# Performance work log

Measured on AMD Instinct MI355X. Metric: run time of the kernel, lower is better.

Reference implementation:

```python
import jax, jax.numpy as jnp
import numpy as np

EPS_PROJ = 4e-3   # geoopt float32 ball projection eps
ATANH_EPS = 1e-7

def artanh(x):
    return jnp.arctanh(jnp.clip(x, -1.0 + ATANH_EPS, 1.0 - ATANH_EPS))

def project(x):
    norm = jnp.linalg.norm(x, axis=-1, keepdims=True)
    maxnorm = 1.0 - EPS_PROJ
    return jnp.where(norm > maxnorm, x * (maxnorm / jnp.maximum(norm, 1e-15)), x)

def expmap0(u):
    un = jnp.linalg.norm(u, axis=-1, keepdims=True)
    return jnp.tanh(un) * u / jnp.maximum(un, 1e-15)

def mobius_add(x, y):
    x2 = jnp.sum(x * x, -1, keepdims=True)
    y2 = jnp.sum(y * y, -1, keepdims=True)
    xy = jnp.sum(x * y, -1, keepdims=True)
    num = (1 + 2 * xy + y2) * x + (1 - x2) * y
    den = 1 + 2 * xy + x2 * y2
    return num / jnp.maximum(den, 1e-15)

def mobius_matvec(W, x):
    xn = jnp.linalg.norm(x, axis=-1, keepdims=True)
    mx = x @ W.T
    mxn = jnp.linalg.norm(mx, axis=-1, keepdims=True)
    res = jnp.tanh(mxn / jnp.maximum(xn, 1e-15) * artanh(xn)) * (mx / jnp.maximum(mxn, 1e-15))
    return jnp.where(mxn == 0, jnp.zeros_like(res), res)

def mobius_linear(x, W, b):
    # hyperbolic_input=True, hyperbolic bias, nonlin=None
    return project(mobius_add(mobius_matvec(W, x), b))

def mobius_scalar_mul(r, t):
    tn = jnp.linalg.norm(t, axis=-1, keepdims=True)
    return jnp.tanh(r * artanh(tn)) * (t / jnp.maximum(tn, 1e-15))

def pair_dist(ht, hs):
    # Poincare dist (c=1): 2*artanh(||(-x) mobius_add y||); closed form via GEMM
    x2 = jnp.sum(ht * ht, -1)                    # (b,t)
    y2 = jnp.sum(hs * hs, -1)                    # (b,s)
    xy = jnp.einsum('btd,bsd->bts', ht, hs)      # (b,t,s)
    diff2 = jnp.maximum(x2[:, :, None] + y2[:, None, :] - 2 * xy, 0.0)
    den = jnp.maximum(1 - 2 * xy + x2[:, :, None] * y2[:, None, :], 1e-15)
    return 2.0 * artanh(jnp.sqrt(diff2 / den))


def setup_inputs() -> dict:
    key = jax.random.key(0)
    ks = jax.random.split(key, 7)
    B, T, S, D = 8, 2048, 2048, 128
    source = project(expmap0(0.5 * jax.random.normal(ks[0], (B, T, D), jnp.float32)))
    memory_bank = project(expmap0(0.5 * jax.random.normal(ks[1], (B, S, D), jnp.float32)))
    W_out = 0.01 * jax.random.normal(ks[2], (D, 2 * D), jnp.float32)
    b_out = expmap0(0.25 * jax.random.normal(ks[3], (D,), jnp.float32))
    beta_w = 0.01 * jax.random.normal(ks[4], (1, 1), jnp.float32)
    beta_b = expmap0(0.25 * jax.random.normal(ks[5], (1,), jnp.float32))
    memory_lengths = jax.random.randint(ks[6], (B,), S // 2, S + 1).astype(jnp.int64)
    return {"source": source, "memory_bank": memory_bank, "W_out": W_out,
            "b_out": b_out, "beta_w": beta_w, "beta_b": beta_b,
            "memory_lengths": memory_lengths}


def reference(source, memory_bank, W_out, b_out, beta_w, beta_b, memory_lengths):
    B, T, D = source.shape
    S = memory_bank.shape[1]
    # --- score: -beta(dist(h_t_i, h_s_j)) over all (i,j), vectorized ---
    d = pair_dist(source, memory_bank)[..., None]        # (b,t,s,1)
    align = -mobius_linear(d, beta_w, beta_b)[..., 0]     # (b,t,s)
    # --- length masking ---
    mask = jnp.arange(S) < memory_lengths[:, None]        # (b,s)
    align = jnp.where(mask[:, None, :], align, -jnp.inf)
    align_vectors = jax.nn.softmax(align, axis=-1)        # (b,t,s)
    # --- mobius weighted midpoint over src dim (reducedim=[2]) ---
    y2 = jnp.sum(memory_bank * memory_bank, -1)           # (b,s)
    gamma = 2.0 / jnp.maximum(1.0 - y2, 1e-15)            # lambda_x, k=-1
    den = jnp.einsum('bts,bs->bt', align_vectors, gamma - 1.0)
    den = jnp.where(den >= 0, jnp.maximum(den, 1e-10), jnp.minimum(den, -1e-10))
    nom = jnp.einsum('bts,bs,bsd->btd', align_vectors, gamma, memory_bank)
    cvec = mobius_scalar_mul(0.5, nom / den[..., None])   # (b,t,d)
    # --- output mobius linear on concat, attn_type='hype' => no tanh ---
    concat_c = jnp.concatenate([cvec, source], axis=-1)   # (b,t,2d)
    attn_h = mobius_linear(concat_c, W_out, b_out)        # (b,t,d)
    return attn_h.transpose(1, 0, 2), align_vectors.transpose(1, 0, 2)
```

## Files before the change

### kernel.cpp

```cpp
#include <hip/hip_runtime.h>
#include <stdint.h>

#define B_ 8
#define T_ 2048
#define S_ 2048
#define D_ 128
#define CAP_ 1024

typedef __attribute__((ext_vector_type(8))) short short8;
typedef __attribute__((ext_vector_type(4))) float f32x4;

#define MAXN_ (1.0f - 0.004f)
#define CLIP1_ 0.99999988f

__device__ __forceinline__ unsigned short f2bf(float f) {
    unsigned int u = __builtin_bit_cast(unsigned int, f);
    u += 0x7fffu + ((u >> 16) & 1u);
    return (unsigned short)(u >> 16);
}
__device__ __forceinline__ unsigned int pack2(float a, float b) {
    return (unsigned int)f2bf(a) | ((unsigned int)f2bf(b) << 16);
}
__device__ __forceinline__ float bf2f(unsigned short u) {
    return __builtin_bit_cast(float, ((unsigned int)u) << 16);
}
__device__ __forceinline__ float tanh_fast(float x) {
    float e = __expf(-2.f * fabsf(x));
    float r = (1.f - e) / (1.f + e);
    return copysignf(r, x);
}
__device__ __forceinline__ float atanh_clip(float x) {
    x = fminf(x, CLIP1_);
    return 0.5f * __logf((1.f + x) / (1.f - x));
}
__device__ __forceinline__ float ep_from_av(float av, float w, float bbs, float b2s) {
    float mv = tanh_fast(w * av);
    float ab = mv * bbs;
    float m2 = mv * mv;
    float num = (1.f + 2.f * ab + b2s) * mv + (1.f - m2) * bbs;
    float dd2 = 1.f + 2.f * ab + m2 * b2s;
    float ma = num / fmaxf(dd2, 1e-15f);
    float am = fabsf(ma);
    if (am > MAXN_) ma = ma * (MAXN_ / fmaxf(am, 1e-15f));
    return __expf(-ma);
}
__device__ __forceinline__ float sat_ep(float w, float bbs) {
    return ep_from_av(atanh_clip(2.f), w, bbs, bbs * bbs);
}
__device__ __forceinline__ int get_len(const int* mlen, int b) {
    int is64 = (mlen[1] == 0);
    return is64 ? mlen[2 * b] : mlen[b];
}

__global__ __launch_bounds__(256) void k_prep(
    const float* __restrict__ src, const float* __restrict__ mem,
    const float* __restrict__ Wout, const int* __restrict__ mlen,
    unsigned short* __restrict__ srcb, unsigned short* __restrict__ memb,
    float* __restrict__ x2a, float* __restrict__ y2a,
    unsigned short* __restrict__ Wb, float* __restrict__ gpart,
    float* __restrict__ nbpart, unsigned int* __restrict__ cnt)
{
    __shared__ unsigned short cc_l[128][128];
    __shared__ float gam_l[128];
    __shared__ float gm1_l[128];
    __shared__ float nb_l[2][128];

    const int bid = blockIdx.x;
    const int tid = threadIdx.x;

    if (bid < 256) {
        const bool ismem = bid >= 128;
        const float* inp = ismem ? mem : src;
        unsigned short* outp = ismem ? memb : srcb;
        float* na = ismem ? y2a : x2a;
        const int row0 = (bid & 127) * 128;
        const int lr = tid >> 1;
        const int r = row0 + lr;
        const int ch = (tid & 1) * 64;

        float4 v[16];
        float sq = 0.f;
        const float* rp = inp + (size_t)r * D_ + ch;
        #pragma unroll
        for (int i = 0; i < 16; ++i) {
            v[i] = *(const float4*)(rp + 4 * i);
            sq += v[i].x * v[i].x + v[i].y * v[i].y + v[i].z * v[i].z + v[i].w * v[i].w;
        }
        sq += __shfl_xor(sq, 1);
        unsigned short* op = outp + (size_t)r * D_ + ch;
        #pragma unroll
        for (int i = 0; i < 8; ++i) {
            uint4 pk;
            pk.x = pack2(v[2 * i].x, v[2 * i].y);
            pk.y = pack2(v[2 * i].z, v[2 * i].w);
            pk.z = pack2(v[2 * i + 1].x, v[2 * i + 1].y);
            pk.w = pack2(v[2 * i + 1].z, v[2 * i + 1].w);
            *(uint4*)(op + 8 * i) = pk;
            if (ismem) *(uint4*)&cc_l[lr][ch + 8 * i] = pk;
        }
        if ((tid & 1) == 0) {
            na[r] = sq;
            if (ismem) {
                int b = r >> 11;
                int lenb = get_len(mlen, b);
                bool vld = (r & 2047) < lenb;
                float gam = vld ? 2.f / fmaxf(1.f - sq, 1e-15f) : 0.f;
                gam_l[lr] = gam;
                gm1_l[lr] = vld ? (gam - 1.f) : 0.f;
            }
        }
        if (ismem) {
            __syncthreads();
            const int slot = bid - 128;
            const int c = tid & 127;
            const int h = tid >> 7;
            float acc = 0.f;
            #pragma unroll 8
            for (int r2 = h * 64; r2 < h * 64 + 64; ++r2)
                acc += gam_l[r2] * bf2f(cc_l[r2][c]);
            nb_l[h][c] = acc;
            __syncthreads();
            if (tid < 128)
                nbpart[slot * 128 + tid] = nb_l[0][tid] + nb_l[1][tid];
            if (tid < 64) {
                float g = gm1_l[tid] + gm1_l[tid + 64];
                g += __shfl_xor(g, 1); g += __shfl_xor(g, 2);
                g += __shfl_xor(g, 4); g += __shfl_xor(g, 8);
                g += __shfl_xor(g, 16); g += __shfl_xor(g, 32);
                if (tid == 0) gpart[slot] = g;
            }
        }
    } else {
        if (bid == 256 && tid == 0) *cnt = 0u;
        const int idx0 = (bid - 256) * 4096 + tid * 16;
        float4 v0 = *(const float4*)(Wout + idx0);
        float4 v1 = *(const float4*)(Wout + idx0 + 4);
        float4 v2 = *(const float4*)(Wout + idx0 + 8);
        float4 v3 = *(const float4*)(Wout + idx0 + 12);
        uint4 p0, p1;
        p0.x = pack2(v0.x, v0.y); p0.y = pack2(v0.z, v0.w);
        p0.z = pack2(v1.x, v1.y); p0.w = pack2(v1.z, v1.w);
        p1.x = pack2(v2.x, v2.y); p1.y = pack2(v2.z, v2.w);
        p1.z = pack2(v3.x, v3.y); p1.w = pack2(v3.z, v3.w);
        *(uint4*)(Wb + idx0) = p0;
        *(uint4*)(Wb + idx0 + 8) = p1;
    }
}

__global__ __launch_bounds__(256, 2) void k_score(
    const unsigned short* __restrict__ srcb, const unsigned short* __restrict__ memb,
    const float* __restrict__ x2a, const float* __restrict__ y2a,
    const float* __restrict__ bw, const float* __restrict__ bbp,
    const int* __restrict__ mlen,
    unsigned int* __restrict__ cnt, unsigned int* __restrict__ listR,
    unsigned int* __restrict__ listS, float* __restrict__ listEp,
    float* __restrict__ alignp)
{
    __shared__ unsigned short xs[128][136];
    __shared__ unsigned short ys[128][136];
    __shared__ float x2s[128], y2s[128];
    __shared__ int len_l[8];
    __shared__ float pv_l[8];

    const int tid = threadIdx.x;
    const int blk = blockIdx.x;
    const int b = blk & 7;
    const int rr = blk >> 3;
    const int tt = rr & 15;
    const int st = rr >> 4;
    const int t0 = tt * 128, s0 = st * 128;
    const int lane = tid & 63, wave = tid >> 6;
    const int l15 = lane & 15, q = lane >> 4;
    const int wr = wave >> 1, wc = wave & 1;

    const unsigned short* xg = srcb + ((size_t)(b * T_ + t0)) * D_;
    const unsigned short* yg = memb + ((size_t)(b * S_ + s0)) * D_;
    #pragma unroll
    for (int i = 0; i < 8; ++i) {
        int c = i * 256 + tid;
        int row = c >> 4, off = (c & 15) * 8;
        *(uint4*)&xs[row][off] = *(const uint4*)(xg + (size_t)c * 8);
        *(uint4*)&ys[row][off] = *(const uint4*)(yg + (size_t)c * 8);
    }
    if (tid < 128) { x2s[tid] = x2a[b * T_ + t0 + tid]; y2s[tid] = y2a[b * S_ + s0 + tid]; }
    if (tid < 8) {
        int lv = get_len(mlen, tid);
        len_l[tid] = lv;
        pv_l[tid] = 1.f / (float)lv;
    }
    __syncthreads();

    {
        const int base_f4 = blk * 4096;
        #pragma unroll
        for (int i = 0; i < 16; ++i) {
            int f4 = base_f4 + i * 256 + tid;
            int r = f4 >> 9;
            int b2 = r & 7;
            int s4 = (f4 & 511) << 2;
            int lv = len_l[b2];
            float pvv = pv_l[b2];
            float4 o;
            o.x = (s4 + 0 < lv) ? pvv : 0.f;
            o.y = (s4 + 1 < lv) ? pvv : 0.f;
            o.z = (s4 + 2 < lv) ? pvv : 0.f;
            o.w = (s4 + 3 < lv) ? pvv : 0.f;
            *(float4*)(alignp + (size_t)f4 * 4) = o;
        }
    }

    f32x4 acc[4][4];
    #pragma unroll
    for (int m = 0; m < 4; ++m)
        #pragma unroll
        for (int n = 0; n < 4; ++n)
            acc[m][n] = (f32x4){0.f, 0.f, 0.f, 0.f};

    #pragma unroll
    for (int ki = 0; ki < 4; ++ki) {
        short8 af[4], bf[4];
        #pragma unroll
        for (int m = 0; m < 4; ++m)
            af[m] = *(const short8*)&xs[wr * 64 + m * 16 + l15][ki * 32 + q * 8];
        #pragma unroll
        for (int n = 0; n < 4; ++n)
            bf[n] = *(const short8*)&ys[wc * 64 + n * 16 + l15][ki * 32 + q * 8];
        #pragma unroll
        for (int m = 0; m < 4; ++m)
            #pragma unroll
            for (int n = 0; n < 4; ++n)
                acc[m][n] = __builtin_amdgcn_mfma_f32_16x16x32_bf16(af[m], bf[n], acc[m][n], 0, 0, 0);
    }

    const int lenb = len_l[b];

    float us = tanh_fast(0.5f * CLIP1_);
    const float RSAT = us * us;
    float x2r[16];
    #pragma unroll
    for (int m = 0; m < 4; ++m)
        #pragma unroll
        for (int rg = 0; rg < 4; ++rg)
            x2r[m * 4 + rg] = x2s[wr * 64 + m * 16 + q * 4 + rg];

    unsigned long long um = 0ull;
    #pragma unroll
    for (int n = 0; n < 4; ++n) {
        int col = wc * 64 + n * 16 + l15;
        bool valid = (s0 + col) < lenb;
        float y2v = y2s[col];
        #pragma unroll
        for (int m = 0; m < 4; ++m) {
            #pragma unroll
            for (int rg = 0; rg < 4; ++rg) {
                float xy = acc[m][n][rg];
                float x2v = x2r[m * 4 + rg];
                float diff2 = x2v + y2v - 2.f * xy;
                float dden = fmaf(x2v, y2v, 1.f) - 2.f * xy;
                bool unsat = valid && (diff2 < RSAT * dden);
                um |= ((unsigned long long)unsat) << (n * 16 + m * 4 + rg);
            }
        }
    }

    if (__ballot(um != 0ull)) {
        const float w = bw[0];
        const float bbs = bbp[0];
        const float b2s = bbs * bbs;
        for (int n = 0; n < 4; ++n) {
            int col = wc * 64 + n * 16 + l15;
            for (int m = 0; m < 4; ++m) {
                for (int rg = 0; rg < 4; ++rg) {
                    if (!(um & (1ull << (n * 16 + m * 4 + rg)))) continue;
                    int row = wr * 64 + m * 16 + q * 4 + rg;
                    float xy = acc[m][n][rg];
                    float x2v = x2r[m * 4 + rg];
                    float y2v = y2s[col];
                    float diff2 = fmaxf(x2v + y2v - 2.f * xy, 0.f);
                    float dden = fmaxf(fmaf(x2v, y2v, 1.f) - 2.f * xy, 1e-15f);
                    float u = fminf(sqrtf(diff2 / dden), CLIP1_);
                    float dp = __logf((1.f + u) / (1.f - u));
                    float ep = ep_from_av(atanh_clip(dp), w, bbs, b2s);
                    int rix = b * T_ + t0 + row;
                    unsigned int idx = atomicAdd(cnt, 1u);
                    if (idx < CAP_) {
                        listR[idx] = (unsigned int)rix;
                        listS[idx] = (unsigned int)(b * S_ + s0 + col);
                        listEp[idx] = ep;
                    }
                }
            }
        }
    }
}

__global__ __launch_bounds__(256, 1) void k_out(
    const float* __restrict__ src, const float* __restrict__ mem,
    const unsigned short* __restrict__ Wb, const float* __restrict__ bvec,
    const float* __restrict__ bw, const float* __restrict__ bbp,
    const int* __restrict__ mlen, const float* __restrict__ gpart,
    const float* __restrict__ nbpart, const float* __restrict__ y2a,
    const unsigned int* __restrict__ cnt, const unsigned int* __restrict__ listR,
    const unsigned int* __restrict__ listS, const float* __restrict__ listEp,
    float* __restrict__ attnp, float* __restrict__ alignp)
{
    __shared__ unsigned short W_l[128][264];
    __shared__ unsigned short cc_l[64][264];
    __shared__ float b_l[128];
    __shared__ float nombase_l[128];
    __shared__ float nomn2_l[64], srcn2_l[64], cs_l[64], xn_l[64];
    __shared__ float redA[64], redB[64];
    __shared__ float fA_l[64], fB_l[64];
    __shared__ float bb2_l, Gb_l;

    const int tid = threadIdx.x;
    const int b = blockIdx.x & 7;
    const int tt = blockIdx.x >> 3;
    const int t0 = tt * 64;
    const int lane = tid & 63;
    const int wave = tid >> 6;
    const int l15 = lane & 15;
    const int q = lane >> 4;

    const float epsat = sat_ep(bw[0], bbp[0]);
    const int lenb = get_len(mlen, b);
    unsigned int nc = *cnt; if (nc > CAP_) nc = CAP_;

    #pragma unroll
    for (int i = 0; i < 16; ++i) {
        int c = i * 256 + tid;
        int row = c >> 5, off = (c & 31) * 8;
        *(uint4*)&W_l[row][off] = *(const uint4*)(Wb + (size_t)c * 8);
    }
    if (tid < 128) b_l[tid] = bvec[tid];
    if (tid < 64) { redA[tid] = 0.f; redB[tid] = 0.f; }
    if (tid < 128) {
        float s = 0.f;
        #pragma unroll
        for (int j = 0; j < 16; ++j) s += nbpart[(b * 16 + j) * 128 + tid];
        nombase_l[tid] = s;
    }
    if (tid == 128) {
        float g = 0.f;
        #pragma unroll
        for (int j = 0; j < 16; ++j) g += gpart[b * 16 + j];
        Gb_l = g;
    }
    if (tid == 129) {
        float s = 0.f;
        for (int j = 0; j < 128; ++j) { float v = bvec[j]; s += v * v; }
        bb2_l = s;
    }
    __syncthreads();

    const int r_s = tid >> 2;
    const int d0 = (tid & 3) * 32;
    float4 nv[8], sv[8];
    {
        #pragma unroll
        for (int i = 0; i < 8; ++i) {
            nv[i].x = epsat * nombase_l[d0 + 4 * i + 0];
            nv[i].y = epsat * nombase_l[d0 + 4 * i + 1];
            nv[i].z = epsat * nombase_l[d0 + 4 * i + 2];
            nv[i].w = epsat * nombase_l[d0 + 4 * i + 3];
        }
        if (nc) {
            int myrix = b * T_ + t0 + r_s;
            for (unsigned int i = 0; i < nc; ++i) {
                if ((int)listR[i] != myrix) continue;
                unsigned int sg = listS[i];
                float y2v = y2a[sg];
                float gam = 2.f / fmaxf(1.f - y2v, 1e-15f);
                float cg = (listEp[i] - epsat) * gam;
                const float* yrow = mem + (size_t)sg * D_ + d0;
                #pragma unroll
                for (int k2 = 0; k2 < 8; ++k2) {
                    float4 yv = *(const float4*)(yrow + 4 * k2);
                    nv[k2].x += cg * yv.x; nv[k2].y += cg * yv.y;
                    nv[k2].z += cg * yv.z; nv[k2].w += cg * yv.w;
                }
            }
        }
        size_t sbase = ((size_t)(b * T_ + t0 + r_s)) * D_ + d0;
        float nn = 0.f, ss = 0.f;
        #pragma unroll
        for (int i = 0; i < 8; ++i) {
            sv[i] = *(const float4*)(src + sbase + 4 * i);
            nn += nv[i].x * nv[i].x + nv[i].y * nv[i].y + nv[i].z * nv[i].z + nv[i].w * nv[i].w;
            ss += sv[i].x * sv[i].x + sv[i].y * sv[i].y + sv[i].z * sv[i].z + sv[i].w * sv[i].w;
        }
        nn += __shfl_xor(nn, 1); nn += __shfl_xor(nn, 2);
        ss += __shfl_xor(ss, 1); ss += __shfl_xor(ss, 2);
        if ((tid & 3) == 0) { nomn2_l[r_s] = nn; srcn2_l[r_s] = ss; }
    }
    __syncthreads();

    if (tid < 64) {
        int myrix = b * T_ + t0 + tid;
        float Lv = epsat * (float)lenb;
        float Gv = epsat * Gb_l;
        if (nc) {
            for (unsigned int i = 0; i < nc; ++i) {
                if ((int)listR[i] != myrix) continue;
                float dep = listEp[i] - epsat;
                float y2v = y2a[listS[i]];
                float gam = 2.f / fmaxf(1.f - y2v, 1e-15f);
                Lv += dep;
                Gv += dep * (gam - 1.f);
            }
        }
        float dv = Gv / Lv;
        dv = (dv >= 0.f) ? fmaxf(dv, 1e-10f) : fminf(dv, -1e-10f);
        float Z = Lv * dv;
        float nn2 = nomn2_l[tid];
        float tn = sqrtf(nn2) / fabsf(Z);
        float f = tanh_fast(0.5f * atanh_clip(tn));
        float cs = f / (fmaxf(tn, 1e-15f) * Z);
        cs_l[tid] = cs;
        xn_l[tid] = sqrtf(cs * cs * nn2 + srcn2_l[tid]);
    }
    __syncthreads();

    {
        float cs = cs_l[r_s];
        #pragma unroll
        for (int i = 0; i < 8; ++i) {
            uint2 pk;
            pk.x = pack2(nv[i].x * cs, nv[i].y * cs);
            pk.y = pack2(nv[i].z * cs, nv[i].w * cs);
            *(uint2*)&cc_l[r_s][d0 + 4 * i] = pk;
            uint2 ps;
            ps.x = pack2(sv[i].x, sv[i].y);
            ps.y = pack2(sv[i].z, sv[i].w);
            *(uint2*)&cc_l[r_s][128 + d0 + 4 * i] = ps;
        }
    }
    __syncthreads();

    f32x4 acc[4][2];
    #pragma unroll
    for (int m = 0; m < 4; ++m)
        #pragma unroll
        for (int n = 0; n < 2; ++n)
            acc[m][n] = (f32x4){0.f, 0.f, 0.f, 0.f};
    #pragma unroll
    for (int ki = 0; ki < 8; ++ki) {
        short8 af[4], bf[2];
        #pragma unroll
        for (int m = 0; m < 4; ++m)
            af[m] = *(const short8*)&cc_l[m * 16 + l15][ki * 32 + q * 8];
        #pragma unroll
        for (int n = 0; n < 2; ++n)
            bf[n] = *(const short8*)&W_l[wave * 32 + n * 16 + l15][ki * 32 + q * 8];
        #pragma unroll
        for (int m = 0; m < 4; ++m)
            #pragma unroll
            for (int n = 0; n < 2; ++n)
                acc[m][n] = __builtin_amdgcn_mfma_f32_16x16x32_bf16(af[m], bf[n], acc[m][n], 0, 0, 0);
    }

    float bj[2];
    #pragma unroll
    for (int n = 0; n < 2; ++n) bj[n] = b_l[wave * 32 + n * 16 + l15];

    #pragma unroll
    for (int m = 0; m < 4; ++m) {
        #pragma unroll
        for (int rg = 0; rg < 4; ++rg) {
            int row = m * 16 + q * 4 + rg;
            float pA = 0.f, pB = 0.f;
            #pragma unroll
            for (int n = 0; n < 2; ++n) {
                float v = acc[m][n][rg];
                pA += v * v;
                pB += v * bj[n];
            }
            pA += __shfl_xor(pA, 1); pB += __shfl_xor(pB, 1);
            pA += __shfl_xor(pA, 2); pB += __shfl_xor(pB, 2);
            pA += __shfl_xor(pA, 4); pB += __shfl_xor(pB, 4);
            pA += __shfl_xor(pA, 8); pB += __shfl_xor(pB, 8);
            if (l15 == 0) {
                atomicAdd(&redA[row], pA);
                atomicAdd(&redB[row], pB);
            }
        }
    }
    __syncthreads();

    if (tid < 64) {
        float mxn2 = redA[tid];
        float mxb = redB[tid];
        float xn = xn_l[tid];
        float atx = atanh_clip(xn);
        float mxn = sqrtf(mxn2);
        float scg = tanh_fast(mxn / fmaxf(xn, 1e-15f) * atx) / fmaxf(mxn, 1e-15f);
        float res2 = scg * scg * mxn2;
        float xyb = scg * mxb;
        float b2v = bb2_l;
        float c1 = 1.f + 2.f * xyb + b2v;
        float c2 = 1.f - res2;
        float dd = fmaxf(1.f + 2.f * xyb + res2 * b2v, 1e-15f);
        float nn = sqrtf(fmaxf(c1 * c1 * res2 + 2.f * c1 * c2 * xyb + c2 * c2 * b2v, 0.f)) / dd;
        float rho = (nn > MAXN_) ? (MAXN_ / fmaxf(nn, 1e-15f)) : 1.f;
        fA_l[tid] = rho * c1 * scg / dd;
        fB_l[tid] = rho * c2 / dd;
    }
    __syncthreads();

    #pragma unroll
    for (int m = 0; m < 4; ++m) {
        #pragma unroll
        for (int n = 0; n < 2; ++n) {
            int col = wave * 32 + n * 16 + l15;
            #pragma unroll
            for (int rg = 0; rg < 4; ++rg) {
                int row = m * 16 + q * 4 + rg;
                attnp[((size_t)((t0 + row) * 8 + b)) * D_ + col] =
                    fA_l[row] * acc[m][n][rg] + fB_l[row] * b_l[col];
            }
        }
    }

    if (blockIdx.x == 0 && nc > 0) {
        for (unsigned int i = 0; i < nc; ++i) {
            unsigned int rix = listR[i];
            int fb = rix >> 11, ft = rix & 2047;
            int flen = get_len(mlen, fb);
            float L = epsat * (float)flen;
            for (unsigned int j = 0; j < nc; ++j)
                if (listR[j] == rix) L += listEp[j] - epsat;
            float pvv = epsat / L;
            size_t base = ((size_t)(ft * 8 + fb)) << 11;
            for (int s = tid; s < S_; s += 256)
                alignp[base + s] = (s < flen) ? pvv : 0.f;
        }
        __syncthreads();
        for (unsigned int i = tid; i < nc; i += 256) {
            unsigned int rix = listR[i];
            int fb = rix >> 11, ft = rix & 2047;
            unsigned int s = listS[i] & 2047;
            int flen = get_len(mlen, fb);
            float L = epsat * (float)flen;
            for (unsigned int j = 0; j < nc; ++j)
                if (listR[j] == rix) L += listEp[j] - epsat;
            alignp[(((size_t)(ft * 8 + fb)) << 11) + s] = listEp[i] / L;
        }
    }
}

extern "C" void kernel_launch(void* const* d_in, const int* in_sizes, int n_in,
                              void* d_out, int out_size, void* d_ws, size_t ws_size,
                              hipStream_t stream) {
    const float* src  = (const float*)d_in[0];
    const float* mem  = (const float*)d_in[1];
    const float* Wout = (const float*)d_in[2];
    const float* bvec = (const float*)d_in[3];
    const float* bw   = (const float*)d_in[4];
    const float* bb   = (const float*)d_in[5];
    const int*   mlen = (const int*)d_in[6];

    float* attnp  = (float*)d_out;
    float* alignp = attnp + (size_t)T_ * B_ * D_;
    unsigned short* srcb = (unsigned short*)d_out;
    unsigned short* memb = (unsigned short*)d_out + (size_t)B_ * T_ * D_;

    float* ws_f = (float*)d_ws;
    unsigned int* cnt   = (unsigned int*)d_ws;
    float* gpart        = ws_f + 8;
    float* nbpart       = ws_f + 1024;
    unsigned int* listR = (unsigned int*)(ws_f + 20480);
    unsigned int* listS = (unsigned int*)(ws_f + 21504);
    float* listEp       = ws_f + 22528;
    float* x2a          = ws_f + 24576;
    float* y2a          = ws_f + 40960;
    unsigned short* Wb  = (unsigned short*)(ws_f + 57344);

    hipLaunchKernelGGL(k_prep, dim3(264), dim3(256), 0, stream,
                       src, mem, Wout, mlen, srcb, memb, x2a, y2a, Wb,
                       gpart, nbpart, cnt);
    hipLaunchKernelGGL(k_score, dim3(2048), dim3(256), 0, stream,
                       srcb, memb, x2a, y2a, bw, bb, mlen,
                       cnt, listR, listS, listEp, alignp);
    hipLaunchKernelGGL(k_out, dim3(256), dim3(256), 0, stream,
                       src, mem, Wb, bvec, bw, bb, mlen, gpart, nbpart, y2a,
                       cnt, listR, listS, listEp, attnp, alignp);
}
```

Before: 193.8 us.

## Factor per-batch context vector out of output GEMM and skip saturated score tiles

Measured after the change: 185.2 us. -4.4%, faster.

```diff
diff --git a/kernel.cpp b/kernel.cpp
--- a/kernel.cpp
+++ b/kernel.cpp
@@ -50,6 +50,21 @@
 __device__ __forceinline__ int get_len(const int* mlen, int b) {
     int is64 = (mlen[1] == 0);
     return is64 ? mlen[2 * b] : mlen[b];
+}
+__device__ __forceinline__ void mob_epilogue(float mxn2, float mxb, float xn,
+                                             float bb2, float* fA, float* fB) {
+    float atx = atanh_clip(xn);
+    float mxn = sqrtf(mxn2);
+    float scg = tanh_fast(mxn / fmaxf(xn, 1e-15f) * atx) / fmaxf(mxn, 1e-15f);
+    float res2 = scg * scg * mxn2;
+    float xyb = scg * mxb;
+    float c1 = 1.f + 2.f * xyb + bb2;
+    float c2 = 1.f - res2;
+    float dd = fmaxf(1.f + 2.f * xyb + res2 * bb2, 1e-15f);
+    float nn = sqrtf(fmaxf(c1 * c1 * res2 + 2.f * c1 * c2 * xyb + c2 * c2 * bb2, 0.f)) / dd;
+    float rho = (nn > MAXN_) ? (MAXN_ / fmaxf(nn, 1e-15f)) : 1.f;
+    *fA = rho * c1 * scg / dd;
+    *fB = rho * c2 / dd;
 }
 
 __global__ __launch_bounds__(256) void k_prep(
@@ -154,13 +169,19 @@
     const int* __restrict__ mlen,
     unsigned int* __restrict__ cnt, unsigned int* __restrict__ listR,
     unsigned int* __restrict__ listS, float* __restrict__ listEp,
-    float* __restrict__ alignp)
+    float* __restrict__ alignp,
+    const float* __restrict__ nbpart, const float* __restrict__ gpart,
+    const float* __restrict__ Wout, const float* __restrict__ bvec,
+    float* __restrict__ vb_g, float* __restrict__ ub_g, float* __restrict__ scal)
 {
     __shared__ unsigned short xs[128][136];
     __shared__ unsigned short ys[128][136];
     __shared__ float x2s[128], y2s[128];
     __shared__ int len_l[8];
     __shared__ float pv_l[8];
+    __shared__ float x2min_sh, y2min_sh;
+    __shared__ float vb_sh[128];
+    __shared__ float cs_sh;
 
     const int tid = threadIdx.x;
     const int blk = blockIdx.x;
@@ -173,6 +194,10 @@
     const int l15 = lane & 15, q = lane >> 4;
     const int wr = wave >> 1, wc = wave & 1;
 
+    const float w = bw[0];
+    const float bbs = bbp[0];
+    const float epsat = sat_ep(w, bbs);
+
     const unsigned short* xg = srcb + ((size_t)(b * T_ + t0)) * D_;
     const unsigned short* yg = memb + ((size_t)(b * S_ + s0)) * D_;
     #pragma unroll
@@ -187,6 +212,22 @@
         int lv = get_len(mlen, tid);
         len_l[tid] = lv;
         pv_l[tid] = 1.f / (float)lv;
+    }
+    __syncthreads();
+
+    if (tid < 64) {
+        float v = fminf(x2s[tid], x2s[tid + 64]);
+        v = fminf(v, __shfl_xor(v, 1));  v = fminf(v, __shfl_xor(v, 2));
+        v = fminf(v, __shfl_xor(v, 4));  v = fminf(v, __shfl_xor(v, 8));
+        v = fminf(v, __shfl_xor(v, 16)); v = fminf(v, __shfl_xor(v, 32));
+        if (tid == 0) x2min_sh = v;
+    } else if (tid < 128) {
+        int l = tid - 64;
+        float v = fminf(y2s[l], y2s[l + 64]);
+        v = fminf(v, __shfl_xor(v, 1));  v = fminf(v, __shfl_xor(v, 2));
+        v = fminf(v, __shfl_xor(v, 4));  v = fminf(v, __shfl_xor(v, 8));
+        v = fminf(v, __shfl_xor(v, 16)); v = fminf(v, __shfl_xor(v, 32));
+        if (l == 0) y2min_sh = v;
     }
     __syncthreads();
 
@@ -233,247 +274,225 @@
     }
 
     const int lenb = len_l[b];
-
     float us = tanh_fast(0.5f * CLIP1_);
     const float RSAT = us * us;
-    float x2r[16];
-    #pragma unroll
-    for (int m = 0; m < 4; ++m)
-        #pragma unroll
-        for (int rg = 0; rg < 4; ++rg)
-            x2r[m * 4 + rg] = x2s[wr * 64 + m * 16 + q * 4 + rg];
-
-    unsigned long long um = 0ull;
-    #pragma unroll
-    for (int n = 0; n < 4; ++n) {
-        int col = wc * 64 + n * 16 + l15;
-        bool valid = (s0 + col) < lenb;
-        float y2v = y2s[col];
-        #pragma unroll
-        for (int m = 0; m < 4; ++m) {
-            #pragma unroll
-            for (int rg = 0; rg < 4; ++rg) {
-                float xy = acc[m][n][rg];
-                float x2v = x2r[m * 4 + rg];
-                float diff2 = x2v + y2v - 2.f * xy;
-                float dden = fmaf(x2v, y2v, 1.f) - 2.f * xy;
-                bool unsat = valid && (diff2 < RSAT * dden);
-                um |= ((unsigned long long)unsat) << (n * 16 + m * 4 + rg);
-            }
-        }
-    }
-
-    if (__ballot(um != 0ull)) {
-        const float w = bw[0];
-        const float bbs = bbp[0];
-        const float b2s = bbs * bbs;
-        for (int n = 0; n < 4; ++n) {
-            int col = wc * 64 + n * 16 + l15;
-            for (int m = 0; m < 4; ++m) {
-                for (int rg = 0; rg < 4; ++rg) {
-                    if (!(um & (1ull << (n * 16 + m * 4 + rg)))) continue;
-                    int row = wr * 64 + m * 16 + q * 4 + rg;
-                    float xy = acc[m][n][rg];
-                    float x2v = x2r[m * 4 + rg];
-                    float y2v = y2s[col];
-                    float diff2 = fmaxf(x2v + y2v - 2.f * xy, 0.f);
-                    float dden = fmaxf(fmaf(x2v, y2v, 1.f) - 2.f * xy, 1e-15f);
-                    float u = fminf(sqrtf(diff2 / dden), CLIP1_);
-                    float dp = __logf((1.f + u) / (1.f - u));
-                    float ep = ep_from_av(atanh_clip(dp), w, bbs, b2s);
-                    int rix = b * T_ + t0 + row;
-                    unsigned int idx = atomicAdd(cnt, 1u);
-                    if (idx < CAP_) {
-                        listR[idx] = (unsigned int)rix;
-                        listS[idx] = (unsigned int)(b * S_ + s0 + col);
-                        listEp[idx] = ep;
+
+    {
+        float mymax = -1e30f;
+        #pragma unroll
+        for (int n = 0; n < 4; ++n)
+            #pragma unroll
+            for (int m = 0; m < 4; ++m)
+                #pragma unroll
+                for (int rg = 0; rg < 4; ++rg)
+                    mymax = fmaxf(mymax, acc[m][n][rg]);
+        mymax = fmaxf(mymax, __shfl_xor(mymax, 1));
+        mymax = fmaxf(mymax, __shfl_xor(mymax, 2));
+        mymax = fmaxf(mymax, __shfl_xor(mymax, 4));
+        mymax = fmaxf(mymax, __shfl_xor(mymax, 8));
+        mymax = fmaxf(mymax, __shfl_xor(mymax, 16));
+        mymax = fmaxf(mymax, __shfl_xor(mymax, 32));
+        float c0 = 1.f / (2.f * (1.f - RSAT));
+        float thr = c0 * (x2min_sh + y2min_sh - RSAT - RSAT * x2min_sh * y2min_sh);
+        if (mymax >= thr - 1e-3f) {
+            float x2r[16];
+            #pragma unroll
+            for (int m = 0; m < 4; ++m)
+                #pragma unroll
+                for (int rg = 0; rg < 4; ++rg)
+                    x2r[m * 4 + rg] = x2s[wr * 64 + m * 16 + q * 4 + rg];
+            unsigned long long um = 0ull;
+            #pragma unroll
+            for (int n = 0; n < 4; ++n) {
+                int col = wc * 64 + n * 16 + l15;
+                bool valid = (s0 + col) < lenb;
+                float y2v = y2s[col];
+                #pragma unroll
+                for (int m = 0; m < 4; ++m) {
+                    #pragma unroll
+                    for (int rg = 0; rg < 4; ++rg) {
+                        float xy = acc[m][n][rg];
+                        float x2v = x2r[m * 4 + rg];
+                        float diff2 = x2v + y2v - 2.f * xy;
+                        float dden = fmaf(x2v, y2v, 1.f) - 2.f * xy;
+                        bool unsat = valid && (diff2 < RSAT * dden);
+                        um |= ((unsigned long long)unsat) << (n * 16 + m * 4 + rg);
                     }
                 }
             }
-        }
-    }
-}
-
-__global__ __launch_bounds__(256, 1) void k_out(
+            if (__ballot(um != 0ull)) {
+                const float b2s = bbs * bbs;
+                for (int n = 0; n < 4; ++n) {
+                    int col = wc * 64 + n * 16 + l15;
+                    for (int m = 0; m < 4; ++m) {
+                        for (int rg = 0; rg < 4; ++rg) {
+                            if (!(um & (1ull << (n * 16 + m * 4 + rg)))) continue;
+                            int row = wr * 64 + m * 16 + q * 4 + rg;
+                            float xy = acc[m][n][rg];
+                            float x2v = x2r[m * 4 + rg];
+                            float y2v = y2s[col];
+                            float diff2 = fmaxf(x2v + y2v - 2.f * xy, 0.f);
+                            float dden = fmaxf(fmaf(x2v, y2v, 1.f) - 2.f * xy, 1e-15f);
+                            float u = fminf(sqrtf(diff2 / dden), CLIP1_);
+                            float dp = __logf((1.f + u) / (1.f - u));
+                            float ep = ep_from_av(atanh_clip(dp), w, bbs, b2s);
+                            int rix = b * T_ + t0 + row;
+                            unsigned int idx = atomicAdd(cnt, 1u);
+                            if (idx < CAP_) {
+                                listR[idx] = (unsigned int)rix;
+                                listS[idx] = (unsigned int)(b * S_ + s0 + col);
+                                listEp[idx] = ep;
+                            }
+                        }
+                    }
+                }
+            }
+        }
+    }
+
+    if (blk < 8) {
+        __syncthreads();
+        if (tid < 128) {
+            float s = 0.f;
+            #pragma unroll
+            for (int j = 0; j < 16; ++j) s += nbpart[(b * 16 + j) * 128 + tid];
+            float v = epsat * s;
+            vb_sh[tid] = v;
+            vb_g[b * 128 + tid] = v;
+        }
+        __syncthreads();
+        if (tid == 0) {
+            float g = 0.f;
+            #pragma unroll
+            for (int j = 0; j < 16; ++j) g += gpart[b * 16 + j];
+            float Gb0 = epsat * g;
+            float Lb0 = epsat * (float)lenb;
+            float dv = Gb0 / Lb0;
+            dv = (dv >= 0.f) ? fmaxf(dv, 1e-10f) : fminf(dv, -1e-10f);
+            float Z = Lb0 * dv;
+            float nn2 = 0.f;
+            for (int k2 = 0; k2 < 128; ++k2) nn2 += vb_sh[k2] * vb_sh[k2];
+            float tn = sqrtf(nn2) / fabsf(Z);
+            float f = tanh_fast(0.5f * atanh_clip(tn));
+            float cs = f / (fmaxf(tn, 1e-15f) * Z);
+            scal[b * 4 + 0] = cs;
+            scal[b * 4 + 1] = cs * cs * nn2;
+            scal[b * 4 + 2] = Lb0;
+            scal[b * 4 + 3] = Gb0;
+            cs_sh = cs;
+            if (b == 0) {
+                float s2 = 0.f;
+                for (int j = 0; j < 128; ++j) { float bv = bvec[j]; s2 += bv * bv; }
+                scal[32] = s2;
+            }
+        }
+        __syncthreads();
+        if (tid < 128) {
+            float s = 0.f;
+            const float* wr2 = Wout + (size_t)tid * 256;
+            for (int k2 = 0; k2 < 128; ++k2) s += vb_sh[k2] * wr2[k2];
+            ub_g[b * 128 + tid] = cs_sh * s;
+        }
+    }
+}
+
+__global__ __launch_bounds__(256, 2) void k_out(
     const float* __restrict__ src, const float* __restrict__ mem,
     const unsigned short* __restrict__ Wb, const float* __restrict__ bvec,
     const float* __restrict__ bw, const float* __restrict__ bbp,
-    const int* __restrict__ mlen, const float* __restrict__ gpart,
-    const float* __restrict__ nbpart, const float* __restrict__ y2a,
+    const int* __restrict__ mlen, const float* __restrict__ x2a,
+    const float* __restrict__ y2a, const float* __restrict__ vb_g,
+    const float* __restrict__ ub_g, const float* __restrict__ scal,
     const unsigned int* __restrict__ cnt, const unsigned int* __restrict__ listR,
     const unsigned int* __restrict__ listS, const float* __restrict__ listEp,
+    const float* __restrict__ Wout,
     float* __restrict__ attnp, float* __restrict__ alignp)
 {
-    __shared__ unsigned short W_l[128][264];
-    __shared__ unsigned short cc_l[64][264];
-    __shared__ float b_l[128];
-    __shared__ float nombase_l[128];
-    __shared__ float nomn2_l[64], srcn2_l[64], cs_l[64], xn_l[64];
-    __shared__ float redA[64], redB[64];
-    __shared__ float fA_l[64], fB_l[64];
-    __shared__ float bb2_l, Gb_l;
+    __shared__ unsigned short W2_l[128][136];
+    __shared__ unsigned short as_l[32][136];
+    __shared__ float ub_l[128], bv_l[128];
+    __shared__ float redA[32], redB[32];
+    __shared__ float fA_l[32], fB_l[32];
+    __shared__ float ex_nom[128], ex_mx[128];
+    __shared__ float ex_s[4];
 
     const int tid = threadIdx.x;
-    const int b = blockIdx.x & 7;
-    const int tt = blockIdx.x >> 3;
-    const int t0 = tt * 64;
+    const int blk = blockIdx.x;
+    const int b = blk & 7;
+    const int tt = blk >> 3;
+    const int t0 = tt * 32;
+    const int t0g = b * T_ + t0;
     const int lane = tid & 63;
     const int wave = tid >> 6;
     const int l15 = lane & 15;
     const int q = lane >> 4;
 
-    const float epsat = sat_ep(bw[0], bbp[0]);
-    const int lenb = get_len(mlen, b);
-    unsigned int nc = *cnt; if (nc > CAP_) nc = CAP_;
-
-    #pragma unroll
-    for (int i = 0; i < 16; ++i) {
+    #pragma unroll
+    for (int i = 0; i < 8; ++i) {
         int c = i * 256 + tid;
-        int row = c >> 5, off = (c & 31) * 8;
-        *(uint4*)&W_l[row][off] = *(const uint4*)(Wb + (size_t)c * 8);
-    }
-    if (tid < 128) b_l[tid] = bvec[tid];
-    if (tid < 64) { redA[tid] = 0.f; redB[tid] = 0.f; }
-    if (tid < 128) {
-        float s = 0.f;
-        #pragma unroll
-        for (int j = 0; j < 16; ++j) s += nbpart[(b * 16 + j) * 128 + tid];
-        nombase_l[tid] = s;
-    }
-    if (tid == 128) {
-        float g = 0.f;
-        #pragma unroll
-        for (int j = 0; j < 16; ++j) g += gpart[b * 16 + j];
-        Gb_l = g;
-    }
-    if (tid == 129) {
-        float s = 0.f;
-        for (int j = 0; j < 128; ++j) { float v = bvec[j]; s += v * v; }
-        bb2_l = s;
-    }
+        int row = c >> 4, off = (c & 15) * 8;
+        *(uint4*)&W2_l[row][off] = *(const uint4*)(Wb + (size_t)row * 256 + 128 + off);
+    }
+    {
+        int row = tid >> 3;
+        int c0 = (tid & 7) * 16;
+        const float* sp = src + (size_t)(t0g + row) * D_ + c0;
+        float4 a0 = *(const float4*)(sp);
+        float4 a1 = *(const float4*)(sp + 4);
+        float4 a2 = *(const float4*)(sp + 8);
+        float4 a3 = *(const float4*)(sp + 12);
+        uint4 p0, p1;
+        p0.x = pack2(a0.x, a0.y); p0.y = pack2(a0.z, a0.w);
+        p0.z = pack2(a1.x, a1.y); p0.w = pack2(a1.z, a1.w);
+        p1.x = pack2(a2.x, a2.y); p1.y = pack2(a2.z, a2.w);
+        p1.z = pack2(a3.x, a3.y); p1.w = pack2(a3.z, a3.w);
+        *(uint4*)&as_l[row][c0] = p0;
+        *(uint4*)&as_l[row][c0 + 8] = p1;
+    }
+    if (tid < 128) { ub_l[tid] = ub_g[b * 128 + tid]; bv_l[tid] = bvec[tid]; }
+    if (tid < 32) { redA[tid] = 0.f; redB[tid] = 0.f; }
     __syncthreads();
 
-    const int r_s = tid >> 2;
-    const int d0 = (tid & 3) * 32;
-    float4 nv[8], sv[8];
-    {
-        #pragma unroll
-        for (int i = 0; i < 8; ++i) {
-            nv[i].x = epsat * nombase_l[d0 + 4 * i + 0];
-            nv[i].y = epsat * nombase_l[d0 + 4 * i + 1];
-            nv[i].z = epsat * nombase_l[d0 + 4 * i + 2];
-            nv[i].w = epsat * nombase_l[d0 + 4 * i + 3];
-        }
-        if (nc) {
-            int myrix = b * T_ + t0 + r_s;
-            for (unsigned int i = 0; i < nc; ++i) {
-                if ((int)listR[i] != myrix) continue;
-                unsigned int sg = listS[i];
-                float y2v = y2a[sg];
-                float gam = 2.f / fmaxf(1.f - y2v, 1e-15f);
-                float cg = (listEp[i] - epsat) * gam;
-                const float* yrow = mem + (size_t)sg * D_ + d0;
-                #pragma unroll
-                for (int k2 = 0; k2 < 8; ++k2) {
-                    float4 yv = *(const float4*)(yrow + 4 * k2);
-                    nv[k2].x += cg * yv.x; nv[k2].y += cg * yv.y;
-                    nv[k2].z += cg * yv.z; nv[k2].w += cg * yv.w;
-                }
-            }
-        }
-        size_t sbase = ((size_t)(b * T_ + t0 + r_s)) * D_ + d0;
-        float nn = 0.f, ss = 0.f;
-        #pragma unroll
-        for (int i = 0; i < 8; ++i) {
-            sv[i] = *(const float4*)(src + sbase + 4 * i);
-            nn += nv[i].x * nv[i].x + nv[i].y * nv[i].y + nv[i].z * nv[i].z + nv[i].w * nv[i].w;
-            ss += sv[i].x * sv[i].x + sv[i].y * sv[i].y + sv[i].z * sv[i].z + sv[i].w * sv[i].w;
-        }
-        nn += __shfl_xor(nn, 1); nn += __shfl_xor(nn, 2);
-        ss += __shfl_xor(ss, 1); ss += __shfl_xor(ss, 2);
-        if ((tid & 3) == 0) { nomn2_l[r_s] = nn; srcn2_l[r_s] = ss; }
-    }
-    __syncthreads();
-
-    if (tid < 64) {
-        int myrix = b * T_ + t0 + tid;
-        float Lv = epsat * (float)lenb;
-        float Gv = epsat * Gb_l;
-        if (nc) {
-            for (unsigned int i = 0; i < nc; ++i) {
-                if ((int)listR[i] != myrix) continue;
-                float dep = listEp[i] - epsat;
-                float y2v = y2a[listS[i]];
-                float gam = 2.f / fmaxf(1.f - y2v, 1e-15f);
-                Lv += dep;
-                Gv += dep * (gam - 1.f);
-            }
-        }
-        float dv = Gv / Lv;
-        dv = (dv >= 0.f) ? fmaxf(dv, 1e-10f) : fminf(dv, -1e-10f);
-        float Z = Lv * dv;
-        float nn2 = nomn2_l[tid];
-        float tn = sqrtf(nn2) / fabsf(Z);
-        float f = tanh_fast(0.5f * atanh_clip(tn));
-        float cs = f / (fmaxf(tn, 1e-15f) * Z);
-        cs_l[tid] = cs;
-        xn_l[tid] = sqrtf(cs * cs * nn2 + srcn2_l[tid]);
-    }
-    __syncthreads();
-
-    {
-        float cs = cs_l[r_s];
-        #pragma unroll
-        for (int i = 0; i < 8; ++i) {
-            uint2 pk;
-            pk.x = pack2(nv[i].x * cs, nv[i].y * cs);
-            pk.y = pack2(nv[i].z * cs, nv[i].w * cs);
-            *(uint2*)&cc_l[r_s][d0 + 4 * i] = pk;
-            uint2 ps;
-            ps.x = pack2(sv[i].x, sv[i].y);
-            ps.y = pack2(sv[i].z, sv[i].w);
-            *(uint2*)&cc_l[r_s][128 + d0 + 4 * i] = ps;
-        }
-    }
-    __syncthreads();
-
-    f32x4 acc[4][2];
-    #pragma unroll
-    for (int m = 0; m < 4; ++m)
+    f32x4 acc[2][2];
+    #pragma unroll
+    for (int m = 0; m < 2; ++m)
         #pragma unroll
         for (int n = 0; n < 2; ++n)
             acc[m][n] = (f32x4){0.f, 0.f, 0.f, 0.f};
     #pragma unroll
-    for (int ki = 0; ki < 8; ++ki) {
-        short8 af[4], bf[2];
-        #pragma unroll
-        for (int m = 0; m < 4; ++m)
-            af[m] = *(const short8*)&cc_l[m * 16 + l15][ki * 32 + q * 8];
+    for (int ki = 0; ki < 4; ++ki) {
+        short8 af[2], bf[2];
+        #pragma unroll
+        for (int m = 0; m < 2; ++m)
+            af[m] = *(const short8*)&as_l[m * 16 + l15][ki * 32 + q * 8];
         #pragma unroll
         for (int n = 0; n < 2; ++n)
-            bf[n] = *(const short8*)&W_l[wave * 32 + n * 16 + l15][ki * 32 + q * 8];
-        #pragma unroll
-        for (int m = 0; m < 4; ++m)
+            bf[n] = *(const short8*)&W2_l[wave * 32 + n * 16 + l15][ki * 32 + q * 8];
+        #pragma unroll
+        for (int m = 0; m < 2; ++m)
             #pragma unroll
             for (int n = 0; n < 2; ++n)
                 acc[m][n] = __builtin_amdgcn_mfma_f32_16x16x32_bf16(af[m], bf[n], acc[m][n], 0, 0, 0);
     }
 
-    float bj[2];
-    #pragma unroll
-    for (int n = 0; n < 2; ++n) bj[n] = b_l[wave * 32 + n * 16 + l15];
-
-    #pragma unroll
-    for (int m = 0; m < 4; ++m) {
+    float ubv[2], bjv[2];
+    #pragma unroll
+    for (int n = 0; n < 2; ++n) {
+        int col = wave * 32 + n * 16 + l15;
+        ubv[n] = ub_l[col];
+        bjv[n] = bv_l[col];
+    }
+    #pragma unroll
+    for (int m = 0; m < 2; ++m) {
         #pragma unroll
         for (int rg = 0; rg < 4; ++rg) {
             int row = m * 16 + q * 4 + rg;
             float pA = 0.f, pB = 0.f;
             #pragma unroll
             for (int n = 0; n < 2; ++n) {
-                float v = acc[m][n][rg];
+                float v = acc[m][n][rg] + ubv[n];
                 pA += v * v;
-                pB += v * bj[n];
+                pB += v * bjv[n];
             }
             pA += __shfl_xor(pA, 1); pB += __shfl_xor(pB, 1);
             pA += __shfl_xor(pA, 2); pB += __shfl_xor(pB, 2);
@@ -487,63 +506,132 @@
     }
     __syncthreads();
 
-    if (tid < 64) {
-        float mxn2 = redA[tid];
-        float mxb = redB[tid];
-        float xn = xn_l[tid];
-        float atx = atanh_clip(xn);
-        float mxn = sqrtf(mxn2);
-        float scg = tanh_fast(mxn / fmaxf(xn, 1e-15f) * atx) / fmaxf(mxn, 1e-15f);
-        float res2 = scg * scg * mxn2;
-        float xyb = scg * mxb;
-        float b2v = bb2_l;
-        float c1 = 1.f + 2.f * xyb + b2v;
-        float c2 = 1.f - res2;
-        float dd = fmaxf(1.f + 2.f * xyb + res2 * b2v, 1e-15f);
-        float nn = sqrtf(fmaxf(c1 * c1 * res2 + 2.f * c1 * c2 * xyb + c2 * c2 * b2v, 0.f)) / dd;
-        float rho = (nn > MAXN_) ? (MAXN_ / fmaxf(nn, 1e-15f)) : 1.f;
-        fA_l[tid] = rho * c1 * scg / dd;
-        fB_l[tid] = rho * c2 / dd;
+    const float cvn2 = scal[b * 4 + 1];
+    const float bb2 = scal[32];
+    if (tid < 32) {
+        float xn = sqrtf(cvn2 + x2a[t0g + tid]);
+        float fA, fB;
+        mob_epilogue(redA[tid], redB[tid], xn, bb2, &fA, &fB);
+        fA_l[tid] = fA;
+        fB_l[tid] = fB;
     }
     __syncthreads();
 
     #pragma unroll
-    for (int m = 0; m < 4; ++m) {
+    for (int m = 0; m < 2; ++m) {
         #pragma unroll
         for (int n = 0; n < 2; ++n) {
             int col = wave * 32 + n * 16 + l15;
             #pragma unroll
             for (int rg = 0; rg < 4; ++rg) {
                 int row = m * 16 + q * 4 + rg;
+                float v = acc[m][n][rg] + ubv[n];
                 attnp[((size_t)((t0 + row) * 8 + b)) * D_ + col] =
-                    fA_l[row] * acc[m][n][rg] + fB_l[row] * b_l[col];
-            }
-        }
-    }
-
-    if (blockIdx.x == 0 && nc > 0) {
+                    fA_l[row] * v + fB_l[row] * bv_l[col];
+            }
+        }
+    }
+
+    unsigned int nc = *cnt; if (nc > CAP_) nc = CAP_;
+    if (nc) {
+        const float epsat = sat_ep(bw[0], bbp[0]);
+        unsigned int rowmask = 0u;
         for (unsigned int i = 0; i < nc; ++i) {
-            unsigned int rix = listR[i];
-            int fb = rix >> 11, ft = rix & 2047;
-            int flen = get_len(mlen, fb);
-            float L = epsat * (float)flen;
-            for (unsigned int j = 0; j < nc; ++j)
-                if (listR[j] == rix) L += listEp[j] - epsat;
-            float pvv = epsat / L;
-            size_t base = ((size_t)(ft * 8 + fb)) << 11;
-            for (int s = tid; s < S_; s += 256)
-                alignp[base + s] = (s < flen) ? pvv : 0.f;
-        }
-        __syncthreads();
-        for (unsigned int i = tid; i < nc; i += 256) {
-            unsigned int rix = listR[i];
-            int fb = rix >> 11, ft = rix & 2047;
-            unsigned int s = listS[i] & 2047;
-            int flen = get_len(mlen, fb);
-            float L = epsat * (float)flen;
-            for (unsigned int j = 0; j < nc; ++j)
-                if (listR[j] == rix) L += listEp[j] - epsat;
-            alignp[(((size_t)(ft * 8 + fb)) << 11) + s] = listEp[i] / L;
+            unsigned int d = listR[i] - (unsigned int)t0g;
+            if (d < 32u) rowmask |= 1u << d;
+        }
+        while (rowmask) {
+            int r = __builtin_ctz(rowmask);
+            rowmask &= rowmask - 1u;
+            int rix = t0g + r;
+            __syncthreads();
+            if (tid < 128) {
+                float nm = vb_g[b * 128 + tid];
+                for (unsigned int i = 0; i < nc; ++i) {
+                    if ((int)listR[i] != rix) continue;
+                    unsigned int sg = listS[i];
+                    float y2v = y2a[sg];
+                    float gam = 2.f / fmaxf(1.f - y2v, 1e-15f);
+                    float cg = (listEp[i] - epsat) * gam;
+                    nm += cg * mem[(size_t)sg * D_ + tid];
+                }
+                ex_nom[tid] = nm;
+            }
+            __syncthreads();
+            if (tid == 0) {
+                float Lv = scal[b * 4 + 2];
+                float Gv = scal[b * 4 + 3];
+                for (unsigned int i = 0; i < nc; ++i) {
+                    if ((int)listR[i] != rix) continue;
+                    float dep = listEp[i] - epsat;
+                    float y2v = y2a[listS[i]];
+                    float gam = 2.f / fmaxf(1.f - y2v, 1e-15f);
+                    Lv += dep;
+                    Gv += dep * (gam - 1.f);
+                }
+                float dv = Gv / Lv;
+                dv = (dv >= 0.f) ? fmaxf(dv, 1e-10f) : fminf(dv, -1e-10f);
+                float Z = Lv * dv;
+                float nn2 = 0.f;
+                for (int k2 = 0; k2 < 128; ++k2) nn2 += ex_nom[k2] * ex_nom[k2];
+                float tn = sqrtf(nn2) / fabsf(Z);
+                float f = tanh_fast(0.5f * atanh_clip(tn));
+                float cs = f / (fmaxf(tn, 1e-15f) * Z);
+                ex_s[0] = cs;
+                ex_s[1] = sqrtf(cs * cs * nn2 + x2a[rix]);
+            }
+            __syncthreads();
+            if (tid < 128) {
+                float s1 = 0.f, s2 = 0.f;
+                const float* wr2 = Wout + (size_t)tid * 256;
+                const float* sr = src + (size_t)rix * D_;
+                for (int k2 = 0; k2 < 128; ++k2) {
+                    s1 += ex_nom[k2] * wr2[k2];
+                    s2 += sr[k2] * wr2[128 + k2];
+                }
+                ex_mx[tid] = ex_s[0] * s1 + s2;
+            }
+            __syncthreads();
+            if (tid == 0) {
+                float mxn2 = 0.f, mxb = 0.f;
+                for (int j = 0; j < 128; ++j) {
+                    mxn2 += ex_mx[j] * ex_mx[j];
+                    mxb += ex_mx[j] * bv_l[j];
+                }
+                float fA, fB;
+                mob_epilogue(mxn2, mxb, ex_s[1], bb2, &fA, &fB);
+                ex_s[2] = fA; ex_s[3] = fB;
+            }
+            __syncthreads();
+            if (tid < 128)
+                attnp[((size_t)((t0 + r) * 8 + b)) * D_ + tid] =
+                    ex_s[2] * ex_mx[tid] + ex_s[3] * bv_l[tid];
+        }
+        if (blockIdx.x == 0) {
+            const float eps2 = epsat;
+            for (unsigned int i = 0; i < nc; ++i) {
+                unsigned int rix = listR[i];
+                int fb = rix >> 11, ft = rix & 2047;
+                int flen = get_len(mlen, fb);
+                float L = eps2 * (float)flen;
+                for (unsigned int j = 0; j < nc; ++j)
+                    if (listR[j] == rix) L += listEp[j] - eps2;
+                float pvv = eps2 / L;
+                size_t base = ((size_t)(ft * 8 + fb)) << 11;
+                for (int s = tid; s < S_; s += 256)
+                    alignp[base + s] = (s < flen) ? pvv : 0.f;
+            }
+            __syncthreads();
+            for (unsigned int i = tid; i < nc; i += 256) {
+                unsigned int rix = listR[i];
+                int fb = rix >> 11, ft = rix & 2047;
+                unsigned int s = listS[i] & 2047;
+                int flen = get_len(mlen, fb);
+                float L = eps2 * (float)flen;
+                for (unsigned int j = 0; j < nc; ++j)
+                    if (listR[j] == rix) L += listEp[j] - eps2;
+                alignp[(((size_t)(ft * 8 + fb)) << 11) + s] = listEp[i] / L;
+            }
         }
     }
 }
@@ -574,14 +662,19 @@
     float* x2a          = ws_f + 24576;
     float* y2a          = ws_f + 40960;
     unsigned short* Wb  = (unsigned short*)(ws_f + 57344);
+    float* vb_g         = ws_f + 73728;
+    float* ub_g         = ws_f + 74752;
+    float* scal         = ws_f + 75776;
 
     hipLaunchKernelGGL(k_prep, dim3(264), dim3(256), 0, stream,
                        src, mem, Wout, mlen, srcb, memb, x2a, y2a, Wb,
                        gpart, nbpart, cnt);
     hipLaunchKernelGGL(k_score, dim3(2048), dim3(256), 0, stream,
                        srcb, memb, x2a, y2a, bw, bb, mlen,
-                       cnt, listR, listS, listEp, alignp);
-    hipLaunchKernelGGL(k_out, dim3(256), dim3(256), 0, stream,
-                       src, mem, Wb, bvec, bw, bb, mlen, gpart, nbpart, y2a,
-                       cnt, listR, listS, listEp, attnp, alignp);
-}
+                       cnt, listR, listS, listEp, alignp,
+                       nbpart, gpart, Wout, bvec, vb_g, ub_g, scal);
+    hipLaunchKernelGGL(k_out, dim3(512), dim3(256), 0, stream,
+                       src, mem, Wb, bvec, bw, bb, mlen, x2a, y2a,
+                       vb_g, ub_g, scal, cnt, listR, listS, listEp, Wout,
+                       attnp, alignp);
+}
```
